# Optimization experiments

Hardware: AMD Instinct MI355X
Metric: run time of the kernel (lower is better)

The kernel has to match this reference:

```python
import jax, jax.numpy as jnp
import numpy as np

RTOL = 0.3  # isclose rtol, atol=0


def _extract_windows(x):
    # x: [B,C,H,W] -> windows [B,C,H-2,W-2,3,3] (kernel 3, stride 1, no pad)
    B, C, H, W = x.shape
    Ho, Wo = H - 2, W - 2
    slabs = [x[:, :, i:i + Ho, j:j + Wo] for i in range(3) for j in range(3)]
    w = jnp.stack(slabs, axis=-1)  # [B,C,Ho,Wo,9]
    return w.reshape(B, C, Ho, Wo, 3, 3)


def setup_inputs() -> dict:
    key = jax.random.key(0)
    x = jax.random.normal(key, (8, 64, 130, 130), dtype=jnp.float32)
    return {"x": x}


def reference(x):
    # RegpPooling2D forward: mode-like pooling over 3x3 windows.
    w = _extract_windows(x)  # [B,C,Ho,Wo,3,3]
    # pad each 3x3 window with zeros to 5x5 (matches F.pad(..., (1,1,1,1), value=0))
    wp = jnp.pad(w, ((0, 0), (0, 0), (0, 0), (0, 0), (1, 1), (1, 1)))
    B, C, Ho, Wo = w.shape[:4]
    p = jnp.zeros((B, C, Ho, Wo), dtype=x.dtype)
    max_counter = jnp.zeros((B, C, Ho, Wo), dtype=x.dtype)
    # sequential 9-step update, identical order to the torch double loop
    for n_i in range(3):
        for n_j in range(3):
            sub = wp[..., n_i:n_i + 3, n_j:n_j + 3]  # [B,C,Ho,Wo,3,3]
            c = w[..., n_i, n_j]                      # center value [B,C,Ho,Wo]
            cb = c[..., None, None]
            # torch.isclose(A, B, rtol, atol=0): |A-B| <= rtol*|B|
            close = jnp.abs(sub - cb) <= RTOL * jnp.abs(cb)
            cnt = jnp.sum(close, axis=(-2, -1)).astype(x.dtype) - 1.0
            gt = cnt > max_counter
            p = jnp.where(gt, c, p)
            max_counter = jnp.where(gt, cnt, max_counter)
            # after the update above, cnt == max_counter also holds when gt was true
            p = jnp.where(cnt == max_counter, (c + p) * 0.5, p)
    return p
```

## Files before the change

kernel.cpp:

```cpp
#include <hip/hip_runtime.h>


#define W_T 8
#define QC (W_T + 2)

__global__ __launch_bounds__(256) void regp_pool_kernel(
    const float* __restrict__ x, float* __restrict__ out) {
    const int tx = blockIdx.x * blockDim.x + threadIdx.x;
    const int jt = tx & 15;
    const int i  = (tx >> 4) & 127;
    const int bc = tx >> 11;
    const int j  = jt * W_T;

    const float* __restrict__ src = x + (size_t)bc * (130 * 130) + i * 130 + j;

    float win[3][QC];
#pragma unroll
    for (int rr = 0; rr < 3; ++rr) {
#pragma unroll
        for (int qq = 0; qq < QC; qq += 2) {
            const float2 v = *reinterpret_cast<const float2*>(src + rr * 130 + qq);
            win[rr][qq]     = v.x;
            win[rr][qq + 1] = v.y;
        }
    }

    int cnt[3][QC][3];

#pragma unroll
    for (int r = 0; r < 3; ++r) {
#pragma unroll
        for (int q = 0; q < QC; ++q) {
            const bool needR = (q <= W_T - 1);
            const bool needA = (q >= 1 && q <= W_T);
            const bool needL = (q >= 2);

            const float c = win[r][q];
            const float t = 0.3f * fabsf(c);

            int sl[3], sa[3], sr_[3];
#pragma unroll
            for (int rr = 0; rr < 3; ++rr) {
                if (rr < r - 1 || rr > r + 1) continue;
                const int bl = (q > 0 && (needL || needA))
                                   ? (int)(fabsf(win[rr][q - 1] - c) <= t) : 0;
                const int bm = (rr == r)
                                   ? 1
                                   : (int)(fabsf(win[rr][q] - c) <= t);
                const int br = (q < QC - 1 && (needR || needA))
                                   ? (int)(fabsf(win[rr][q + 1] - c) <= t) : 0;
                if (needR || needA) sr_[rr] = bm + br;
                if (needL)          sl[rr]  = bl + bm;
                if (needA)          sa[rr]  = bl + bm + br;
            }

            int cr = -1, ca = -1, cl = -1;
#pragma unroll
            for (int rr = 0; rr < 3; ++rr) {
                if (rr < r - 1 || rr > r + 1) continue;
                if (needR) cr += sr_[rr];
                if (needA) ca += sa[rr];
                if (needL) cl += sl[rr];
            }

            const int zb = (c == 0.0f) ? 1 : 0;
            if (needR) { const int np = (r == 1) ? 3 : 5; cnt[r][q][0] = cr + np * zb; }
            if (needA) { const int np = (r == 1) ? 0 : 3; cnt[r][q][1] = ca + np * zb; }
            if (needL) { const int np = (r == 1) ? 3 : 5; cnt[r][q][2] = cl + np * zb; }
        }
    }

    float res[W_T];
#pragma unroll
    for (int w = 0; w < W_T; ++w) {
        float p = 0.0f;
        int   mc = 0;
#pragma unroll
        for (int r = 0; r < 3; ++r) {
#pragma unroll
            for (int nj = 0; nj < 3; ++nj) {
                const int   q  = w + nj;
                const float c  = win[r][q];
                const int   cv = cnt[r][q][nj];
                const bool  gt = cv > mc;
                const float pn = gt ? c : p;
                const int  mcn = gt ? cv : mc;
                p  = (cv == mcn) ? (c + pn) * 0.5f : pn;
                mc = mcn;
            }
        }
        res[w] = p;
    }

    float4 o0, o1;
    o0.x = res[0]; o0.y = res[1]; o0.z = res[2]; o0.w = res[3];
    o1.x = res[4]; o1.y = res[5]; o1.z = res[6]; o1.w = res[7];
    float* op = out + (size_t)tx * W_T;
    *reinterpret_cast<float4*>(op)     = o0;
    *reinterpret_cast<float4*>(op + 4) = o1;
}

extern "C" void kernel_launch(void* const* d_in, const int* in_sizes, int n_in,
                              void* d_out, int out_size, void* d_ws, size_t ws_size,
                              hipStream_t stream) {
    const float* x   = (const float*)d_in[0];
    float*       out = (float*)d_out;
    const int threads = 256;
    const int blocks  = (out_size / W_T + threads - 1) / threads;
    regp_pool_kernel<<<blocks, threads, 0, stream>>>(x, out);
}
```

Measured before the change: 35.93 us.

## Compute two output rows per thread sharing comparisons across overlapping windows

Each thread now produces a 2x8 output tile from a 4-row input window instead of 1x8 from 3 rows. The pairwise closeness comparisons of each centre pixel are computed once and reused by both output rows, and the running mode update is applied inline instead of storing a count array first. This halves the thread count, cuts redundant global loads and comparisons, and removes the large per-thread count array. In exchange, the per-thread live state (two sets of p and max counter) grows, which may raise register pressure.

```diff
diff --git a/kernel.cpp b/kernel.cpp
--- a/kernel.cpp
+++ b/kernel.cpp
@@ -8,15 +8,16 @@
     const float* __restrict__ x, float* __restrict__ out) {
     const int tx = blockIdx.x * blockDim.x + threadIdx.x;
     const int jt = tx & 15;
-    const int i  = (tx >> 4) & 127;
-    const int bc = tx >> 11;
+    const int it = (tx >> 4) & 63;
+    const int bc = tx >> 10;
+    const int i  = it * 2;
     const int j  = jt * W_T;
 
     const float* __restrict__ src = x + (size_t)bc * (130 * 130) + i * 130 + j;
 
-    float win[3][QC];
+    float win[4][QC];
 #pragma unroll
-    for (int rr = 0; rr < 3; ++rr) {
+    for (int rr = 0; rr < 4; ++rr) {
 #pragma unroll
         for (int qq = 0; qq < QC; qq += 2) {
             const float2 v = *reinterpret_cast<const float2*>(src + rr * 130 + qq);
@@ -25,79 +26,91 @@
         }
     }
 
-    int cnt[3][QC][3];
+    float p[2][W_T];
+    int   mc[2][W_T];
+#pragma unroll
+    for (int w = 0; w < W_T; ++w) {
+        p[0][w] = 0.0f; p[1][w] = 0.0f;
+        mc[0][w] = 0;   mc[1][w] = 0;
+    }
+
+    auto upd = [](float& pp, int& mm, float c, int cv) {
+        const bool  gt  = cv > mm;
+        const float pn  = gt ? c : pp;
+        const int   mcn = gt ? cv : mm;
+        pp = (cv == mcn) ? (c + pn) * 0.5f : pn;
+        mm = mcn;
+    };
 
 #pragma unroll
-    for (int r = 0; r < 3; ++r) {
+    for (int a = 0; a < 4; ++a) {
 #pragma unroll
         for (int q = 0; q < QC; ++q) {
+            const float c = win[a][q];
+            const float t = 0.3f * fabsf(c);
             const bool needR = (q <= W_T - 1);
             const bool needA = (q >= 1 && q <= W_T);
             const bool needL = (q >= 2);
 
-            const float c = win[r][q];
-            const float t = 0.3f * fabsf(c);
-
-            int sl[3], sa[3], sr_[3];
+            int s[3][3];
 #pragma unroll
-            for (int rr = 0; rr < 3; ++rr) {
-                if (rr < r - 1 || rr > r + 1) continue;
-                const int bl = (q > 0 && (needL || needA))
-                                   ? (int)(fabsf(win[rr][q - 1] - c) <= t) : 0;
-                const int bm = (rr == r)
-                                   ? 1
-                                   : (int)(fabsf(win[rr][q] - c) <= t);
-                const int br = (q < QC - 1 && (needR || needA))
-                                   ? (int)(fabsf(win[rr][q + 1] - c) <= t) : 0;
-                if (needR || needA) sr_[rr] = bm + br;
-                if (needL)          sl[rr]  = bl + bm;
-                if (needA)          sa[rr]  = bl + bm + br;
+            for (int da = -1; da <= 1; ++da) {
+                const int a2 = a + da;
+                if (a2 < 0 || a2 > 3) continue;
+                const bool useW0 = (a <= 2) && (a == 1 || (a == 0 ? (da >= 0) : (da <= 0)));
+                const bool useW1 = (a >= 1) && (a == 2 || (a == 1 ? (da >= 0) : (da <= 0)));
+                if (!(useW0 || useW1)) continue;
+                const int bl = (needA || needL)
+                                   ? (int)(fabsf(win[a2][q - 1] - c) <= t) : 0;
+                const int bm = (da == 0) ? 1
+                                         : (int)(fabsf(win[a2][q] - c) <= t);
+                const int br = (needA || needR)
+                                   ? (int)(fabsf(win[a2][q + 1] - c) <= t) : 0;
+                if (needR) s[0][da + 1] = bm + br;
+                if (needA) s[1][da + 1] = bl + bm + br;
+                if (needL) s[2][da + 1] = bl + bm;
             }
 
-            int cr = -1, ca = -1, cl = -1;
+            const bool zc = (c == 0.0f);
+            const int corr3 = zc ? 2 : -1;
+            const int corr5 = zc ? 4 : -1;
+
 #pragma unroll
-            for (int rr = 0; rr < 3; ++rr) {
-                if (rr < r - 1 || rr > r + 1) continue;
-                if (needR) cr += sr_[rr];
-                if (needA) ca += sa[rr];
-                if (needL) cl += sl[rr];
+            for (int nj = 0; nj < 3; ++nj) {
+                const bool valid = (nj == 0) ? needR : (nj == 1) ? needA : needL;
+                if (!valid) continue;
+                const int px = q - nj;
+
+                if (a == 0) {
+                    const int S = s[nj][1] + s[nj][2];
+                    upd(p[0][px], mc[0][px], c, S + ((nj == 1) ? corr3 : corr5));
+                } else if (a == 1) {
+                    const int T = s[nj][1] + s[nj][2];
+                    upd(p[0][px], mc[0][px], c,
+                        T + s[nj][0] + ((nj == 1) ? -1 : corr3));
+                    upd(p[1][px], mc[1][px], c, T + ((nj == 1) ? corr3 : corr5));
+                } else if (a == 2) {
+                    const int T = s[nj][0] + s[nj][1];
+                    upd(p[0][px], mc[0][px], c, T + ((nj == 1) ? corr3 : corr5));
+                    upd(p[1][px], mc[1][px], c,
+                        T + s[nj][2] + ((nj == 1) ? -1 : corr3));
+                } else {
+                    const int S = s[nj][0] + s[nj][1];
+                    upd(p[1][px], mc[1][px], c, S + ((nj == 1) ? corr3 : corr5));
+                }
             }
-
-            const int zb = (c == 0.0f) ? 1 : 0;
-            if (needR) { const int np = (r == 1) ? 3 : 5; cnt[r][q][0] = cr + np * zb; }
-            if (needA) { const int np = (r == 1) ? 0 : 3; cnt[r][q][1] = ca + np * zb; }
-            if (needL) { const int np = (r == 1) ? 3 : 5; cnt[r][q][2] = cl + np * zb; }
         }
     }
 
-    float res[W_T];
+    float* dst = out + (size_t)bc * (128 * 128) + i * 128 + j;
 #pragma unroll
-    for (int w = 0; w < W_T; ++w) {
-        float p = 0.0f;
-        int   mc = 0;
-#pragma unroll
-        for (int r = 0; r < 3; ++r) {
-#pragma unroll
-            for (int nj = 0; nj < 3; ++nj) {
-                const int   q  = w + nj;
-                const float c  = win[r][q];
-                const int   cv = cnt[r][q][nj];
-                const bool  gt = cv > mc;
-                const float pn = gt ? c : p;
-                const int  mcn = gt ? cv : mc;
-                p  = (cv == mcn) ? (c + pn) * 0.5f : pn;
-                mc = mcn;
-            }
-        }
-        res[w] = p;
+    for (int r2 = 0; r2 < 2; ++r2) {
+        float4 oa, ob;
+        oa.x = p[r2][0]; oa.y = p[r2][1]; oa.z = p[r2][2]; oa.w = p[r2][3];
+        ob.x = p[r2][4]; ob.y = p[r2][5]; ob.z = p[r2][6]; ob.w = p[r2][7];
+        *reinterpret_cast<float4*>(dst + r2 * 128)     = oa;
+        *reinterpret_cast<float4*>(dst + r2 * 128 + 4) = ob;
     }
-
-    float4 o0, o1;
-    o0.x = res[0]; o0.y = res[1]; o0.z = res[2]; o0.w = res[3];
-    o1.x = res[4]; o1.y = res[5]; o1.z = res[6]; o1.w = res[7];
-    float* op = out + (size_t)tx * W_T;
-    *reinterpret_cast<float4*>(op)     = o0;
-    *reinterpret_cast<float4*>(op + 4) = o1;
 }
 
 extern "C" void kernel_launch(void* const* d_in, const int* in_sizes, int n_in,
@@ -106,6 +119,7 @@
     const float* x   = (const float*)d_in[0];
     float*       out = (float*)d_out;
     const int threads = 256;
-    const int blocks  = (out_size / W_T + threads - 1) / threads;
+    const int total_threads = out_size / (2 * W_T);
+    const int blocks  = total_threads / threads;
     regp_pool_kernel<<<blocks, threads, 0, stream>>>(x, out);
 }
```

Result: faster. 32.45 us (-9.7%).
